# Kernel tuning notes

Measured on AMD Instinct MI355X. Metric: run time of the kernel, lower is better.

## Reference

```python
import jax, jax.numpy as jnp
import numpy as np

B, T, V, H = 64, 1024, 512, 512


def setup_inputs() -> dict:
    key = jax.random.key(0)
    ks = jax.random.split(key, 10)
    s = 0.01
    return {
        "X": jax.random.normal(ks[0], (B, T, V), dtype=jnp.float32),
        "state": jnp.zeros((B, H), dtype=jnp.float32),
        "candidate": jnp.zeros((B, H), dtype=jnp.float32),
        "w_xf": jax.random.normal(ks[1], (V, H), dtype=jnp.float32) * s,
        "w_hf": jax.random.normal(ks[2], (H, H), dtype=jnp.float32) * s,
        "b_f": jnp.zeros((H,), dtype=jnp.float32),
        "w_xi": jax.random.normal(ks[3], (V, H), dtype=jnp.float32) * s,
        "w_hi": jax.random.normal(ks[4], (H, H), dtype=jnp.float32) * s,
        "b_i": jnp.zeros((H,), dtype=jnp.float32),
        "w_xo": jax.random.normal(ks[5], (V, H), dtype=jnp.float32) * s,
        "w_ho": jax.random.normal(ks[6], (H, H), dtype=jnp.float32) * s,
        "b_o": jnp.zeros((H,), dtype=jnp.float32),
        "w_xc": jax.random.normal(ks[7], (V, H), dtype=jnp.float32) * s,
        "w_hc": jax.random.normal(ks[8], (H, H), dtype=jnp.float32) * s,
        "b_c": jnp.zeros((H,), dtype=jnp.float32),
        "w_hy": jax.random.normal(ks[9], (H, V), dtype=jnp.float32) * s,
        "b_y": jnp.zeros((V,), dtype=jnp.float32),
    }


def reference(X, state, candidate, w_xf, w_hf, b_f, w_xi, w_hi, b_i,
              w_xo, w_ho, b_o, w_xc, w_hc, b_c, w_hy, b_y):
    # Precompute input projections for all timesteps (same math as per-step mm).
    # Shapes: [T, B, H] (time-major for scan).
    xf = jnp.einsum('btv,vh->tbh', X, w_xf) + b_f
    xi = jnp.einsum('btv,vh->tbh', X, w_xi) + b_i
    xo = jnp.einsum('btv,vh->tbh', X, w_xo) + b_o
    xc = jnp.einsum('btv,vh->tbh', X, w_xc) + b_c

    def step(carry, gates):
        h, c = carry
        gf, gi, go, gc = gates
        f = jax.nn.sigmoid(gf + h @ w_hf)
        i = jax.nn.sigmoid(gi + h @ w_hi)
        o = jax.nn.sigmoid(go + h @ w_ho)
        c_hat = jnp.tanh(gc + h @ w_hc)
        c = f * c + i * c_hat
        h = o * jnp.tanh(c)
        y = h @ w_hy + b_y
        return (h, c), y

    (h_final, c_final), ys = jax.lax.scan(step, (state, candidate), (xf, xi, xo, xc))
    # torch.cat(outputs, dim=0) stacks timesteps along batch dim -> [T*B, V]
    outputs = ys.reshape(T * B, V)
    return outputs, h_final, c_final
```

## Files before the change

kernel.cpp:

```cpp
#include <hip/hip_runtime.h>
#include <hip/hip_bf16.h>
#include <stdint.h>

#define T_STEPS 1024
#define BATCH 64
#define HID 512
#define VOC 512
#define TBV (T_STEPS*BATCH*VOC)
#define POISON 0x7FC17FC1u

typedef __attribute__((ext_vector_type(8))) short bf16x8;
typedef __attribute__((ext_vector_type(8))) unsigned short u16x8;
typedef __attribute__((ext_vector_type(4))) float f32x4;
typedef __attribute__((ext_vector_type(4))) unsigned u32x4;
typedef __attribute__((ext_vector_type(2))) unsigned u32x2;

__device__ __forceinline__ float bf2f(unsigned short u){
  union { unsigned i; float f; } x; x.i = ((unsigned)u)<<16; return x.f;
}
__device__ __forceinline__ unsigned short f2bf(float f){
  union { float f; unsigned i; } x; x.f = f;
  unsigned r = (x.i + 0x7fffu + ((x.i>>16)&1u))>>16;
  return (unsigned short)r;
}
__device__ __forceinline__ float sigm(float x){ return 1.0f/(1.0f+__expf(-x)); }
__device__ __forceinline__ float tanhfast(float x){
  float e = __expf(2.0f*x); return 1.0f - 2.0f/(e+1.0f);
}

__global__ __launch_bounds__(256) void k_pack_x(const float* __restrict__ X,
                                                unsigned short* __restrict__ Xb){
  int idx = blockIdx.x*256 + threadIdx.x;
  int m = idx >> 6, c = idx & 63;
  int b = m & 63, t = m >> 6;
  const float* src = X + ((size_t)b*T_STEPS + t)*VOC + c*8;
  u16x8 v;
  #pragma unroll
  for (int j=0;j<8;j++) v[j] = f2bf(src[j]);
  *(u16x8*)(Xb + (size_t)m*VOC + c*8) = v;
}

__global__ __launch_bounds__(256) void k_pack_wx(const float* __restrict__ wf,
                                                 const float* __restrict__ wi,
                                                 const float* __restrict__ wo,
                                                 const float* __restrict__ wc,
                                                 unsigned short* __restrict__ Wx4t){
  int idx = blockIdx.x*256 + threadIdx.x;
  int n = idx >> 6, c = idx & 63;
  const float* w = (n<512)?wf:(n<1024)?wi:(n<1536)?wo:wc;
  int h = n & 511;
  u16x8 v;
  #pragma unroll
  for (int j=0;j<8;j++) v[j] = f2bf(w[(size_t)(c*8+j)*HID + h]);
  *(u16x8*)(Wx4t + (size_t)n*HID + c*8) = v;
}

__global__ __launch_bounds__(256) void k_pack_wh(const float* __restrict__ whf,
                                                 const float* __restrict__ whi,
                                                 const float* __restrict__ who,
                                                 const float* __restrict__ whc,
                                                 const float* __restrict__ why,
                                                 unsigned short* __restrict__ Wt){
  int idx = blockIdx.x*256 + threadIdx.x;
  int mat = idx >> 15;
  int rem = idx & 32767;
  int col = rem >> 6, c = rem & 63;
  const float* w = (mat==0)?whf:(mat==1)?whi:(mat==2)?who:(mat==3)?whc:why;
  u16x8 v;
  #pragma unroll
  for (int j=0;j<8;j++) v[j] = f2bf(w[(size_t)(c*8+j)*HID + col]);
  *(u16x8*)(Wt + ((size_t)mat*HID + col)*HID + c*8) = v;
}

__global__ __launch_bounds__(256) void k_poison(unsigned* __restrict__ ring){
  size_t i = ((size_t)blockIdx.x*256 + threadIdx.x)*16;
  u32x4 v = {POISON, POISON, POISON, POISON};
  asm volatile("global_store_dwordx4 %0, %1, off sc0 sc1"
               :: "v"((char*)ring + i), "v"(v) : "memory");
}

__global__ __launch_bounds__(256) void k_init_h(const float* __restrict__ state,
                                                unsigned short* __restrict__ ring){
  int idx = blockIdx.x*256 + threadIdx.x;
  int row = idx >> 6, col8 = idx & 63;
  int gt = col8 >> 1, hf = col8 & 1;
  const float* src = state + (size_t)row*HID + col8*8;
  union { unsigned short us[8]; u32x4 v; } u;
  #pragma unroll
  for (int j=0;j<8;j++) u.us[j] = f2bf(src[j]);
  char* dst = (char*)ring + (((size_t)gt*64 + row)*16 + hf*8)*2;
  asm volatile("global_store_dwordx4 %0, %1, off sc0 sc1"
               :: "v"(dst), "v"(u.v) : "memory");
}

__global__ __launch_bounds__(256) void k_gemm_xg(const unsigned short* __restrict__ Xb,
                                                 const unsigned short* __restrict__ Wx4t,
                                                 unsigned short* __restrict__ XG2){
  __shared__ unsigned short Al[128*64];
  __shared__ unsigned short Bl[128*64];
  int tid = threadIdx.x;
  int bid = blockIdx.x;
  int bn = bid & 15, bm = bid >> 4;
  int lane = tid & 63, w = tid >> 6;
  int wm = w >> 1, wn = w & 1;
  int l15 = lane & 15, l4 = lane >> 4;

  f32x4 zero = {0.f,0.f,0.f,0.f};
  f32x4 acc[4][4];
  #pragma unroll
  for (int mi=0;mi<4;mi++)
    #pragma unroll
    for (int ni=0;ni<4;ni++) acc[mi][ni] = zero;

  for (int bk=0; bk<8; ++bk){
    if (bk) __syncthreads();
    #pragma unroll
    for (int it=0; it<4; ++it){
      int L = it*4096 + tid*16;
      int r = L >> 7, ow = L & 127;
      int sw = ow ^ ((r&7)<<4);
      u16x8 va = *(const u16x8*)((const char*)Xb   + (size_t)(bm*128 + r)*1024 + bk*128 + ow);
      u16x8 vb = *(const u16x8*)((const char*)Wx4t + (size_t)(bn*128 + r)*1024 + bk*128 + ow);
      *(u16x8*)((char*)Al + r*128 + sw) = va;
      *(u16x8*)((char*)Bl + r*128 + sw) = vb;
    }
    __syncthreads();
    #pragma unroll
    for (int kt=0; kt<2; ++kt){
      int kb = kt*64 + 16*l4;
      bf16x8 af[4], bfr[4];
      #pragma unroll
      for (int mi=0;mi<4;mi++){
        int r = wm*64 + mi*16 + l15;
        af[mi] = *(const bf16x8*)((const char*)Al + r*128 + (kb ^ ((r&7)<<4)));
      }
      #pragma unroll
      for (int ni=0;ni<4;ni++){
        int r = wn*64 + ni*16 + l15;
        bfr[ni] = *(const bf16x8*)((const char*)Bl + r*128 + (kb ^ ((r&7)<<4)));
      }
      #pragma unroll
      for (int mi=0;mi<4;mi++)
        #pragma unroll
        for (int ni=0;ni<4;ni++)
          acc[mi][ni] = __builtin_amdgcn_mfma_f32_16x16x32_bf16(af[mi], bfr[ni], acc[mi][ni], 0,0,0);
    }
  }
  int t0 = bm*2 + wm;
  #pragma unroll
  for (int mi=0;mi<4;mi++){
    #pragma unroll
    for (int ni=0;ni<4;ni++){
      int col = bn*128 + wn*64 + ni*16;
      int gate = col >> 9, gg = (col >> 4) & 31;
      size_t base = (((size_t)t0*4 + mi)*32 + gg)*1024 + (size_t)gate*256 + l15;
      #pragma unroll
      for (int rr=0;rr<4;rr++)
        XG2[base + (size_t)(l4*4+rr)*16] = f2bf(acc[mi][ni][rr]);
    }
  }
}

__global__ __launch_bounds__(320) void k_scan(
  const unsigned short* __restrict__ XG2, const unsigned short* __restrict__ Wt,
  unsigned short* __restrict__ ring,
  const float* __restrict__ cand,
  const float* __restrict__ b_f, const float* __restrict__ b_i,
  const float* __restrict__ b_o, const float* __restrict__ b_c,
  const float* __restrict__ b_y,
  float* __restrict__ out)
{
  __shared__ char h_lds[16*1024];
  __shared__ float gate_lds[4][16][20];
  int tid = threadIdx.x;
  int w = tid >> 6, lane = tid & 63;
  int l15 = lane & 15, l4 = lane >> 4;
  int grp = blockIdx.x >> 5, g = blockIdx.x & 31;
  int colbase = g*16, rowbase = grp*16;

  u32x4 breg[16];
  {
    const char* wb = (const char*)Wt + ((size_t)(w*HID + colbase + l15))*HID*2 + l4*16;
    #pragma unroll
    for (int kt=0; kt<16; ++kt)
      asm volatile("global_load_dwordx4 %0, %1, off" : "=v"(breg[kt]) : "v"(wb + kt*64));
    asm volatile("s_waitcnt vmcnt(0)" ::: "memory");
    __builtin_amdgcn_sched_barrier(0);
  }

  int cr = tid >> 4, cc = tid & 15;
  int colg = colbase + cc, browg = rowbase + cr;
  float c_val = 0.f, bfv=0.f, biv=0.f, bov=0.f, bcv=0.f;
  if (tid < 256){
    c_val = cand[(size_t)browg*HID + colg];
    bfv = b_f[colg]; biv = b_i[colg]; bov = b_o[colg]; bcv = b_c[colg];
  }
  float byv = (w==4) ? b_y[colbase + l15] : 0.f;

  int rr = (tid>>1) & 15, hf = tid & 1;
  int g0 = tid >> 5;
  int off32[4], ldsw[4]; bool ownj[4];
  #pragma unroll
  for (int j=0;j<4;j++){
    int gj = g0 + 8*j;
    off32[j] = gj*2048 + (rowbase+rr)*32 + hf*16;
    ldsw[j]  = rr*1024 + ((gj*32 + hf*16) ^ ((rr&7)<<4));
    ownj[j]  = (gj == g);
  }

  unsigned short xgf=0, xgi=0, xgo=0, xgc=0;
  if (tid < 256){
    const unsigned short* x0 = XG2 + ((size_t)grp*32 + g)*1024;
    xgf = x0[tid]; xgi = x0[256+tid]; xgo = x0[512+tid]; xgc = x0[768+tid];
  }

  for (int t=0; t<=T_STEPS; ++t){
    const char* rt = (const char*)ring + (size_t)t*65536;
    if (tid < 256){
      const char* p0 = rt + off32[0];
      const char* p1 = rt + off32[1];
      const char* p2 = rt + off32[2];
      const char* p3 = rt + off32[3];
      u32x4 h0, h1, h2, h3;
      for (;;){
        asm volatile(
          "global_load_dwordx4 %0, %4, off sc0 sc1\n\t"
          "global_load_dwordx4 %1, %5, off sc0 sc1\n\t"
          "global_load_dwordx4 %2, %6, off sc0 sc1\n\t"
          "global_load_dwordx4 %3, %7, off sc0 sc1\n\t"
          "s_waitcnt vmcnt(0)"
          : "=&v"(h0), "=&v"(h1), "=&v"(h2), "=&v"(h3)
          : "v"(p0), "v"(p1), "v"(p2), "v"(p3)
          : "memory");
        bool ok = true;
        if (!(ownj[0] && t>0)) ok &= (h0[0]!=POISON)&(h0[1]!=POISON)&(h0[2]!=POISON)&(h0[3]!=POISON);
        if (!(ownj[1] && t>0)) ok &= (h1[0]!=POISON)&(h1[1]!=POISON)&(h1[2]!=POISON)&(h1[3]!=POISON);
        if (!(ownj[2] && t>0)) ok &= (h2[0]!=POISON)&(h2[1]!=POISON)&(h2[2]!=POISON)&(h2[3]!=POISON);
        if (!(ownj[3] && t>0)) ok &= (h3[0]!=POISON)&(h3[1]!=POISON)&(h3[2]!=POISON)&(h3[3]!=POISON);
        if (ok) break;
        __builtin_amdgcn_s_sleep(1);
      }
      if (!(ownj[0] && t>0)) *(u32x4*)(h_lds + ldsw[0]) = h0;
      if (!(ownj[1] && t>0)) *(u32x4*)(h_lds + ldsw[1]) = h1;
      if (!(ownj[2] && t>0)) *(u32x4*)(h_lds + ldsw[2]) = h2;
      if (!(ownj[3] && t>0)) *(u32x4*)(h_lds + ldsw[3]) = h3;
    }
    __syncthreads();

    unsigned short xfn=xgf, xin=xgi, xon=xgo, xcn=xgc;
    if (t+1 < T_STEPS && tid < 256){
      const unsigned short* xn = XG2 + (((size_t)(t+1)*4 + grp)*32 + g)*1024;
      xfn = xn[tid]; xin = xn[256+tid]; xon = xn[512+tid]; xcn = xn[768+tid];
    }

    f32x4 acc0 = {0.f,0.f,0.f,0.f}, acc1 = {0.f,0.f,0.f,0.f};
    #pragma unroll
    for (int kt=0; kt<16; kt+=2){
      bf16x8 a0 = *(const bf16x8*)(h_lds + l15*1024 + (((kt  )*64 + l4*16) ^ ((l15&7)<<4)));
      bf16x8 a1 = *(const bf16x8*)(h_lds + l15*1024 + (((kt+1)*64 + l4*16) ^ ((l15&7)<<4)));
      acc0 = __builtin_amdgcn_mfma_f32_16x16x32_bf16(a0, __builtin_bit_cast(bf16x8, breg[kt]),   acc0, 0,0,0);
      acc1 = __builtin_amdgcn_mfma_f32_16x16x32_bf16(a1, __builtin_bit_cast(bf16x8, breg[kt+1]), acc1, 0,0,0);
    }
    f32x4 accv = acc0 + acc1;

    if (w < 4){
      if (t < T_STEPS){
        #pragma unroll
        for (int r=0;r<4;r++) gate_lds[w][l4*4+r][l15] = accv[r];
      }
    } else if (t >= 1){
      #pragma unroll
      for (int r=0;r<4;r++)
        out[((size_t)(t-1)*64 + rowbase + l4*4 + r)*VOC + colbase + l15] = accv[r] + byv;
    }
    __syncthreads();

    if (t < T_STEPS && tid < 256){
      float gf = bf2f(xgf) + bfv + gate_lds[0][cr][cc];
      float gi = bf2f(xgi) + biv + gate_lds[1][cr][cc];
      float go = bf2f(xgo) + bov + gate_lds[2][cr][cc];
      float gc = bf2f(xgc) + bcv + gate_lds[3][cr][cc];
      float fv = sigm(gf), iv = sigm(gi), ov = sigm(go);
      c_val = fv*c_val + iv*tanhfast(gc);
      float hvf = ov*tanhfast(c_val);
      unsigned hb16 = f2bf(hvf);
      *(unsigned short*)(h_lds + cr*1024 + ((g*32 + cc*2) ^ ((cr&7)<<4))) = (unsigned short)hb16;
      char* hp = (char*)ring + (size_t)(t+1)*65536 + g*2048 + (rowbase+cr)*32 + cc*2;
      asm volatile("global_store_short %0, %1, off sc0 sc1"
                   :: "v"(hp), "v"(hb16) : "memory");
      if (t == T_STEPS-1){
        out[(size_t)TBV + (size_t)browg*512 + colg] = hvf;
        out[(size_t)TBV + 32768 + (size_t)browg*512 + colg] = c_val;
      }
    }
    xgf = xfn; xgi = xin; xgo = xon; xgc = xcn;
  }
}

extern "C" void kernel_launch(void* const* d_in, const int* in_sizes, int n_in,
                              void* d_out, int out_size, void* d_ws, size_t ws_size,
                              hipStream_t stream){
  const float* X    = (const float*)d_in[0];
  const float* state= (const float*)d_in[1];
  const float* cand = (const float*)d_in[2];
  const float* w_xf = (const float*)d_in[3];
  const float* w_hf = (const float*)d_in[4];
  const float* b_f  = (const float*)d_in[5];
  const float* w_xi = (const float*)d_in[6];
  const float* w_hi = (const float*)d_in[7];
  const float* b_i  = (const float*)d_in[8];
  const float* w_xo = (const float*)d_in[9];
  const float* w_ho = (const float*)d_in[10];
  const float* b_o  = (const float*)d_in[11];
  const float* w_xc = (const float*)d_in[12];
  const float* w_hc = (const float*)d_in[13];
  const float* b_c  = (const float*)d_in[14];
  const float* w_hy = (const float*)d_in[15];
  const float* b_y  = (const float*)d_in[16];
  float* out = (float*)d_out;

  char* ws = (char*)d_ws;
  unsigned short* XG2  = (unsigned short*)(ws);
  unsigned short* Xb   = (unsigned short*)(ws + 268435456);
  unsigned short* ring = (unsigned short*)(ws + 268435456);
  unsigned short* Wx4t = (unsigned short*)(ws + 335609856);
  unsigned short* Wt   = (unsigned short*)(ws + 337707008);

  k_pack_x <<<16384,256,0,stream>>>(X, Xb);
  k_pack_wx<<<  512,256,0,stream>>>(w_xf,w_xi,w_xo,w_xc, Wx4t);
  k_pack_wh<<<  640,256,0,stream>>>(w_hf,w_hi,w_ho,w_hc,w_hy, Wt);
  k_gemm_xg<<< 8192,256,0,stream>>>(Xb, Wx4t, XG2);
  k_poison <<<16400,256,0,stream>>>((unsigned*)ring);
  k_init_h <<<   16,256,0,stream>>>(state, ring);
  k_scan   <<<  128,320,0,stream>>>(XG2, Wt, ring, cand, b_f,b_i,b_o,b_c,b_y, out);
}
```

Measured before the change: 2.157 ms.

## Move output projection out of recurrent scan into separate batched GEMM kernel

Removes the fifth wave that computed y = h@w_hy inside the serial scan loop. Each block now runs 256 threads with four gate waves only. A new k_gemm_y kernel computes all outputs afterwards from the h history stored in the ring buffer, using 1024 blocks. This shortens the per-step critical path of the latency-bound recurrence and moves the output GEMM into a fully parallel pass. The cost is an extra kernel launch and rereading h from global memory.

New measurement: 2.324 ms (median of 2 runs). 1.08x slower.

```diff
diff --git a/kernel.cpp b/kernel.cpp
--- a/kernel.cpp
+++ b/kernel.cpp
@@ -13,7 +13,6 @@
 typedef __attribute__((ext_vector_type(8))) unsigned short u16x8;
 typedef __attribute__((ext_vector_type(4))) float f32x4;
 typedef __attribute__((ext_vector_type(4))) unsigned u32x4;
-typedef __attribute__((ext_vector_type(2))) unsigned u32x2;
 
 __device__ __forceinline__ float bf2f(unsigned short u){
   union { unsigned i; float f; } x; x.i = ((unsigned)u)<<16; return x.f;
@@ -161,13 +160,15 @@
   }
 }
 
-__global__ __launch_bounds__(320) void k_scan(
+#define SB() __builtin_amdgcn_sched_barrier(0)
+#define BC(X) __builtin_bit_cast(bf16x8, X)
+
+__global__ __launch_bounds__(256,1) void k_scan(
   const unsigned short* __restrict__ XG2, const unsigned short* __restrict__ Wt,
   unsigned short* __restrict__ ring,
   const float* __restrict__ cand,
   const float* __restrict__ b_f, const float* __restrict__ b_i,
   const float* __restrict__ b_o, const float* __restrict__ b_c,
-  const float* __restrict__ b_y,
   float* __restrict__ out)
 {
   __shared__ char h_lds[16*1024];
@@ -185,17 +186,13 @@
     for (int kt=0; kt<16; ++kt)
       asm volatile("global_load_dwordx4 %0, %1, off" : "=v"(breg[kt]) : "v"(wb + kt*64));
     asm volatile("s_waitcnt vmcnt(0)" ::: "memory");
-    __builtin_amdgcn_sched_barrier(0);
+    SB();
   }
 
   int cr = tid >> 4, cc = tid & 15;
   int colg = colbase + cc, browg = rowbase + cr;
-  float c_val = 0.f, bfv=0.f, biv=0.f, bov=0.f, bcv=0.f;
-  if (tid < 256){
-    c_val = cand[(size_t)browg*HID + colg];
-    bfv = b_f[colg]; biv = b_i[colg]; bov = b_o[colg]; bcv = b_c[colg];
-  }
-  float byv = (w==4) ? b_y[colbase + l15] : 0.f;
+  float c_val = cand[(size_t)browg*HID + colg];
+  float bfv = b_f[colg], biv = b_i[colg], bov = b_o[colg], bcv = b_c[colg];
 
   int rr = (tid>>1) & 15, hf = tid & 1;
   int g0 = tid >> 5;
@@ -208,15 +205,15 @@
     ownj[j]  = (gj == g);
   }
 
-  unsigned short xgf=0, xgi=0, xgo=0, xgc=0;
-  if (tid < 256){
+  unsigned short xgf, xgi, xgo, xgc;
+  {
     const unsigned short* x0 = XG2 + ((size_t)grp*32 + g)*1024;
     xgf = x0[tid]; xgi = x0[256+tid]; xgo = x0[512+tid]; xgc = x0[768+tid];
   }
 
-  for (int t=0; t<=T_STEPS; ++t){
+  for (int t=0; t<T_STEPS; ++t){
     const char* rt = (const char*)ring + (size_t)t*65536;
-    if (tid < 256){
+    {
       const char* p0 = rt + off32[0];
       const char* p1 = rt + off32[1];
       const char* p2 = rt + off32[2];
@@ -248,7 +245,7 @@
     __syncthreads();
 
     unsigned short xfn=xgf, xin=xgi, xon=xgo, xcn=xgc;
-    if (t+1 < T_STEPS && tid < 256){
+    if (t+1 < T_STEPS){
       const unsigned short* xn = XG2 + (((size_t)(t+1)*4 + grp)*32 + g)*1024;
       xfn = xn[tid]; xin = xn[256+tid]; xon = xn[512+tid]; xcn = xn[768+tid];
     }
@@ -258,24 +255,16 @@
     for (int kt=0; kt<16; kt+=2){
       bf16x8 a0 = *(const bf16x8*)(h_lds + l15*1024 + (((kt  )*64 + l4*16) ^ ((l15&7)<<4)));
       bf16x8 a1 = *(const bf16x8*)(h_lds + l15*1024 + (((kt+1)*64 + l4*16) ^ ((l15&7)<<4)));
-      acc0 = __builtin_amdgcn_mfma_f32_16x16x32_bf16(a0, __builtin_bit_cast(bf16x8, breg[kt]),   acc0, 0,0,0);
-      acc1 = __builtin_amdgcn_mfma_f32_16x16x32_bf16(a1, __builtin_bit_cast(bf16x8, breg[kt+1]), acc1, 0,0,0);
+      acc0 = __builtin_amdgcn_mfma_f32_16x16x32_bf16(a0, BC(breg[kt]),   acc0, 0,0,0);
+      acc1 = __builtin_amdgcn_mfma_f32_16x16x32_bf16(a1, BC(breg[kt+1]), acc1, 0,0,0);
     }
     f32x4 accv = acc0 + acc1;
 
-    if (w < 4){
-      if (t < T_STEPS){
-        #pragma unroll
-        for (int r=0;r<4;r++) gate_lds[w][l4*4+r][l15] = accv[r];
-      }
-    } else if (t >= 1){
-      #pragma unroll
-      for (int r=0;r<4;r++)
-        out[((size_t)(t-1)*64 + rowbase + l4*4 + r)*VOC + colbase + l15] = accv[r] + byv;
-    }
+    #pragma unroll
+    for (int r=0;r<4;r++) gate_lds[w][l4*4+r][l15] = accv[r];
     __syncthreads();
 
-    if (t < T_STEPS && tid < 256){
+    {
       float gf = bf2f(xgf) + bfv + gate_lds[0][cr][cc];
       float gi = bf2f(xgi) + biv + gate_lds[1][cr][cc];
       float go = bf2f(xgo) + bov + gate_lds[2][cr][cc];
@@ -294,6 +283,49 @@
       }
     }
     xgf = xfn; xgi = xin; xgo = xon; xgc = xcn;
+  }
+}
+
+__global__ __launch_bounds__(256) void k_gemm_y(
+  const unsigned short* __restrict__ ring, const unsigned short* __restrict__ Wt,
+  const float* __restrict__ b_y, float* __restrict__ out)
+{
+  int tid = threadIdx.x;
+  int w = tid >> 6, lane = tid & 63;
+  int l15 = lane & 15, l4 = lane >> 4;
+  size_t s = (size_t)blockIdx.x + 1;
+
+  u32x4 fa[16];
+  {
+    const char* rb = (const char*)ring + s*65536
+                   + (size_t)((l4>>1)*2048 + (w*16 + l15)*32 + (l4&1)*16);
+    #pragma unroll
+    for (int kt=0;kt<16;++kt)
+      asm volatile("global_load_dwordx4 %0, %1, off sc0 sc1"
+                   : "=v"(fa[kt]) : "v"(rb + (size_t)kt*4096));
+    asm volatile("s_waitcnt vmcnt(0)" ::: "memory");
+    SB();
+  }
+
+  const char* wyb = (const char*)Wt + (size_t)(4*512 + l15)*1024 + l4*16;
+  size_t orow = ((size_t)(s-1)*64 + w*16 + l4*4)*VOC;
+
+  for (int nt=0; nt<32; ++nt){
+    bf16x8 bfrag[16];
+    #pragma unroll
+    for (int kt=0;kt<16;++kt)
+      bfrag[kt] = *(const bf16x8*)(wyb + (size_t)nt*16384 + (size_t)kt*64);
+    f32x4 a0 = {0.f,0.f,0.f,0.f}, a1 = a0;
+    #pragma unroll
+    for (int kt=0;kt<16;kt+=2){
+      a0 = __builtin_amdgcn_mfma_f32_16x16x32_bf16(BC(fa[kt]),   bfrag[kt],   a0, 0,0,0);
+      a1 = __builtin_amdgcn_mfma_f32_16x16x32_bf16(BC(fa[kt+1]), bfrag[kt+1], a1, 0,0,0);
+    }
+    f32x4 accv = a0 + a1;
+    float byv = b_y[nt*16 + l15];
+    #pragma unroll
+    for (int r=0;r<4;++r)
+      out[orow + (size_t)r*VOC + nt*16 + l15] = accv[r] + byv;
   }
 }
 
@@ -332,5 +364,6 @@
   k_gemm_xg<<< 8192,256,0,stream>>>(Xb, Wx4t, XG2);
   k_poison <<<16400,256,0,stream>>>((unsigned*)ring);
   k_init_h <<<   16,256,0,stream>>>(state, ring);
-  k_scan   <<<  128,320,0,stream>>>(XG2, Wt, ring, cand, b_f,b_i,b_o,b_c,b_y, out);
-}
+  k_scan   <<<  128,256,0,stream>>>(XG2, Wt, ring, cand, b_f,b_i,b_o,b_c, out);
+  k_gemm_y <<<1024,256,0,stream>>>(ring, Wt, b_y, out);
+}
```
